# Performance work log

Measured on AMD Instinct MI355X. Metric: run time of the kernel, lower is better.

## Reference

```python
import jax, jax.numpy as jnp
import numpy as np

H, N, L = 512, 64, 2048


def setup_inputs() -> dict:
    key = jax.random.key(0)
    ks = jax.random.split(key, 9)
    x = jax.random.normal(ks[0], (L, H), jnp.float32)
    # HiPPO-style diagonal-plus-low-rank init (stable: Re(Lambda) < 0)
    lambda_re = -0.5 * jnp.ones((N,), jnp.float32)
    lambda_im = jnp.pi * jnp.arange(N, dtype=jnp.float32)
    p_re = jax.random.normal(ks[1], (N,), jnp.float32) / np.sqrt(2 * N)
    p_im = jax.random.normal(ks[2], (N,), jnp.float32) / np.sqrt(2 * N)
    b_re = jax.random.normal(ks[3], (N,), jnp.float32)
    b_im = jax.random.normal(ks[4], (N,), jnp.float32)
    c_re = jax.random.normal(ks[5], (N,), jnp.float32)
    c_im = jax.random.normal(ks[6], (N,), jnp.float32)
    log_step = jnp.array(np.log(0.01), jnp.float32)
    w1 = jax.random.normal(ks[7], (H, H), jnp.float32) / np.sqrt(H)
    bias1 = jnp.zeros((H,), jnp.float32)
    w2 = jax.random.normal(ks[8], (H, H), jnp.float32) / np.sqrt(H)
    bias2 = jnp.zeros((H,), jnp.float32)
    return dict(x=x, lambda_re=lambda_re, lambda_im=lambda_im, p_re=p_re, p_im=p_im,
                b_re=b_re, b_im=b_im, c_re=c_re, c_im=c_im, log_step=log_step,
                w1=w1, bias1=bias1, w2=w2, bias2=bias2)


def _discrete_dplr(Lam, P, B, C, step, seq_len):
    # Bilinear discretization of the DPLR SSM A = diag(Lam) - P P^* (annotated-S4).
    n = Lam.shape[0]
    I = jnp.eye(n, dtype=jnp.complex64)
    A = jnp.diag(Lam) - P[:, None] * jnp.conj(P)[None, :]
    A0 = (2.0 / step) * I + A
    Dd = jnp.diag(1.0 / (2.0 / step - Lam))  # (2/dt - Lam)^{-1} diagonal
    Qc = jnp.conj(P)[None, :]                 # (1, N)
    P2 = P[:, None]                           # (N, 1)
    A1 = Dd - (Dd @ P2) @ (Qc @ Dd) / (1.0 + (Qc @ Dd @ P2))  # Woodbury
    Ab = A1 @ A0                               # (N, N) discrete transition
    Bb = 2.0 * (A1 @ B[:, None])[:, 0]         # (N,)
    Cb = jnp.conj(
        C[None, :] @ jnp.conj(jnp.linalg.inv(I - jnp.linalg.matrix_power(Ab, seq_len)))
    )[0]                                       # (N,)
    return Ab, Bb, Cb


def reference(x, lambda_re, lambda_im, p_re, p_im, b_re, b_im, c_re, c_im,
              log_step, w1, bias1, w2, bias2):
    seq_len, hidden = x.shape
    Lam = (lambda_re + 1j * lambda_im).astype(jnp.complex64)
    P = (p_re + 1j * p_im).astype(jnp.complex64)
    B = (b_re + 1j * b_im).astype(jnp.complex64)
    C = (c_re + 1j * c_im).astype(jnp.complex64)
    step = jnp.exp(log_step)
    Ab, Bb, Cb = _discrete_dplr(Lam, P, B, C, step, seq_len)

    skip = x
    state0 = jnp.zeros((hidden, Lam.shape[0]), jnp.complex64)  # (H, N)

    def step_fn(state, u_l):  # u_l: (H,) real inputs at one timestep
        state = state @ Ab.T + u_l[:, None] * Bb[None, :]  # (H, N)
        y = (state @ Cb).real                               # (H,)
        return state, y

    _, ys = jax.lax.scan(step_fn, state0, x)  # ys: (L, H)
    h = jax.nn.gelu(ys)
    out = (h @ w1.T + bias1) * jax.nn.sigmoid(h @ w2.T + bias2)
    return skip + out
```

## Files before the change

### kernel.cpp

```cpp
#include <hip/hip_runtime.h>
#include <hip/hip_bf16.h>

typedef unsigned short u16;
typedef short s16x8 __attribute__((ext_vector_type(8)));
typedef u16 u16x8 __attribute__((ext_vector_type(8)));
typedef unsigned int u32x4 __attribute__((ext_vector_type(4)));
typedef float f32x4 __attribute__((ext_vector_type(4)));

struct cplx { float x, y; };

#define L_SEQ 2048
#define HID 512
#define NST 64

__device__ __align__(16) cplx g_khat[L_SEQ];
__device__ __align__(16) float g_k[L_SEQ];
__device__ __align__(16) u16 g_T[L_SEQ * L_SEQ];
__device__ __align__(16) u16 g_Xt[HID * L_SEQ];
__device__ __align__(16) u16 g_W1[HID * HID];
__device__ __align__(16) u16 g_W2[HID * HID];
__device__ __align__(16) u16 g_H[L_SEQ * HID];

__device__ __forceinline__ u16 f2bf(float f) {
    union { __hip_bfloat16 h; u16 u; } cv;
    cv.h = __float2bfloat16(f);
    return cv.u;
}

__global__ __launch_bounds__(256) void khat_kernel(
    const float* lre, const float* lim, const float* pre, const float* pim,
    const float* bre, const float* bim, const float* cre, const float* cim,
    const float* lstep) {
    __shared__ float sLre[NST], sLim[NST], sPre[NST], sPim[NST];
    __shared__ float sBre[NST], sBim[NST], sCre[NST], sCim[NST];
    int tid = threadIdx.x;
    if (tid < NST) {
        sLre[tid] = lre[tid]; sLim[tid] = lim[tid];
        sPre[tid] = pre[tid]; sPim[tid] = pim[tid];
        sBre[tid] = bre[tid]; sBim[tid] = bim[tid];
        sCre[tid] = cre[tid]; sCim[tid] = cim[tid];
    }
    __syncthreads();
    int j = blockIdx.x * 256 + tid;
    float tdt = 2.0f * __expf(-lstep[0]);
    float th = 0.00306796157577128245f * j;
    float sn, cs;
    __sincosf(th, &sn, &cs);
    float aRe = tdt * (1.f - cs), aIm = tdt * sn;
    float bRe = 1.f + cs, bIm = -sn;
    float cBx = 0.f, cBy = 0.f, cPx = 0.f, cPy = 0.f;
    float pBx = 0.f, pBy = 0.f, pPx = 0.f, pPy = 0.f;
#pragma unroll 8
    for (int n = 0; n < NST; n++) {
        float Lre = sLre[n], Lim = sLim[n];
        float Dre = aRe - (bRe * Lre - bIm * Lim);
        float Dim = aIm - (bRe * Lim + bIm * Lre);
        float inv = 1.f / (Dre * Dre + Dim * Dim);
        float eRe = Dre * inv, eIm = -Dim * inv;
        float cRe = sCre[n], cIm = -sCim[n];
        float t1Re = cRe * eRe - cIm * eIm, t1Im = cRe * eIm + cIm * eRe;
        float qRe = sPre[n], qIm = -sPim[n];
        float t2Re = qRe * eRe - qIm * eIm, t2Im = qRe * eIm + qIm * eRe;
        float BRe = sBre[n], BIm = sBim[n], PRe = sPre[n], PIm = sPim[n];
        cBx += t1Re * BRe - t1Im * BIm; cBy += t1Re * BIm + t1Im * BRe;
        cPx += t1Re * PRe - t1Im * PIm; cPy += t1Re * PIm + t1Im * PRe;
        pBx += t2Re * BRe - t2Im * BIm; pBy += t2Re * BIm + t2Im * BRe;
        pPx += t2Re * PRe - t2Im * PIm; pPy += t2Re * PIm + t2Im * PRe;
    }
    float denx = 1.f + (bRe * pPx - bIm * pPy);
    float deny = (bRe * pPy + bIm * pPx);
    float bcPx = bRe * cPx - bIm * cPy;
    float bcPy = bRe * cPy + bIm * cPx;
    float numx = bcPx * pBx - bcPy * pBy;
    float numy = bcPx * pBy + bcPy * pBx;
    float dinv = 1.f / (denx * denx + deny * deny);
    float corx = (numx * denx + numy * deny) * dinv;
    float cory = (numy * denx - numx * deny) * dinv;
    g_khat[j] = { 2.f * (cBx - corx), 2.f * (cBy - cory) };
}

__global__ __launch_bounds__(256) void k_ifft() {
    int tid = threadIdx.x;
    int l = tid & 63;
    int t = blockIdx.x * 4 + (tid >> 6);
    float acc = 0.f;
#pragma unroll
    for (int i = 0; i < 16; i++) {
        int j = l + 64 * i;
        cplx a = g_khat[j];
        cplx b = g_khat[(2048 - j) & 2047];
        float re = 0.5f * (a.x + b.x);
        float im = 0.5f * (a.y - b.y);
        int idx = (j * t) & 2047;
        float s, c;
        __sincosf(0.00306796157577128245f * idx, &s, &c);
        float wgt = (j == 0) ? 1.f : 2.f;
        acc += wgt * (re * c - im * s);
    }
    if (l == 0) {
        acc += (1 - 2 * (t & 1)) * g_khat[1024].x;
    }
#pragma unroll
    for (int off = 1; off < 64; off <<= 1) acc += __shfl_xor(acc, off);
    if (l == 0) g_k[t] = acc * (1.f / 2048.f);
}

__global__ __launch_bounds__(256) void fused_convert(const float* x, const float* w1,
                                                     const float* w2) {
    __shared__ float tile[64][65];
    int b = blockIdx.x, tid = threadIdx.x;
    if (b < 256) {
        int lt = b >> 3, ht = b & 7;
#pragma unroll
        for (int i = 0; i < 16; i++) {
            int idx = i * 256 + tid;
            int rr = idx >> 6, cc = idx & 63;
            tile[rr][cc] = x[(lt * 64 + rr) * HID + ht * 64 + cc];
        }
        __syncthreads();
#pragma unroll
        for (int i = 0; i < 16; i++) {
            int idx = i * 256 + tid;
            int rr = idx >> 6, cc = idx & 63;
            g_Xt[(ht * 64 + rr) * L_SEQ + lt * 64 + cc] = f2bf(tile[cc][rr]);
        }
    } else if (b < 768) {
        int t = (b - 256) * 256 + tid;
        const float* src = (t < 65536) ? w1 : w2;
        u16* dst = (t < 65536) ? g_W1 : g_W2;
        int idx = (t < 65536) ? t : (t - 65536);
        float4 v = ((const float4*)src)[idx];
        unsigned long long pk = (unsigned long long)f2bf(v.x) |
                                ((unsigned long long)f2bf(v.y) << 16) |
                                ((unsigned long long)f2bf(v.z) << 32) |
                                ((unsigned long long)f2bf(v.w) << 48);
        ((unsigned long long*)dst)[idx] = pk;
    } else {
        int gid = (b - 768) * 256 + tid;
        int o = gid * 8;
        int i = o >> 11, j0 = o & 2047;
        u16x8 v;
#pragma unroll
        for (int q = 0; q < 8; q++) {
            int d = i - (j0 + q);
            v[q] = f2bf((d >= 0) ? g_k[d] : 0.f);
        }
        *(u16x8*)&g_T[o] = v;
    }
}

__global__ __launch_bounds__(256) void conv_gemm() {
    __shared__ __align__(16) u16 As[64 * 64];
    __shared__ __align__(16) u16 Bs[64 * 64];
    int tid = threadIdx.x, l = tid & 63, w = tid >> 6;
    int wm = w >> 1, wn = w & 1;
    int bm = blockIdx.x >> 3, bn = blockIdx.x & 7;
    f32x4 acc[2][2] = {};
    int nkb = bm + 1;
    int row0 = tid >> 3, kc0 = tid & 7;
    int row1 = (256 + tid) >> 3, kc1 = tid & 7;
    const u16* arow0 = &g_T[(bm * 64 + row0) * L_SEQ + kc0 * 8];
    const u16* arow1 = &g_T[(bm * 64 + row1) * L_SEQ + kc1 * 8];
    const u16* brow0 = &g_Xt[(bn * 64 + row0) * L_SEQ + kc0 * 8];
    const u16* brow1 = &g_Xt[(bn * 64 + row1) * L_SEQ + kc1 * 8];
    int sa0 = row0 * 8 + (kc0 ^ (row0 & 7));
    int sa1 = row1 * 8 + (kc1 ^ (row1 & 7));
    u32x4 ra0 = *(const u32x4*)arow0;
    u32x4 ra1 = *(const u32x4*)arow1;
    u32x4 rb0 = *(const u32x4*)brow0;
    u32x4 rb1 = *(const u32x4*)brow1;
    for (int kb = 0; kb < nkb; kb++) {
        __syncthreads();
        ((u32x4*)As)[sa0] = ra0;
        ((u32x4*)As)[sa1] = ra1;
        ((u32x4*)Bs)[sa0] = rb0;
        ((u32x4*)Bs)[sa1] = rb1;
        if (kb + 1 < nkb) {
            int k0 = (kb + 1) * 64;
            ra0 = *(const u32x4*)(arow0 + k0);
            ra1 = *(const u32x4*)(arow1 + k0);
            rb0 = *(const u32x4*)(brow0 + k0);
            rb1 = *(const u32x4*)(brow1 + k0);
        }
        __syncthreads();
#pragma unroll
        for (int ks = 0; ks < 2; ks++) {
            s16x8 af[2], bf[2];
#pragma unroll
            for (int m = 0; m < 2; m++) {
                int row = wm * 32 + m * 16 + (l & 15);
                int chunk = (ks * 4 + (l >> 4)) ^ (row & 7);
                af[m] = *(const s16x8*)&As[row * 64 + chunk * 8];
            }
#pragma unroll
            for (int n = 0; n < 2; n++) {
                int col = wn * 32 + n * 16 + (l & 15);
                int chunk = (ks * 4 + (l >> 4)) ^ (col & 7);
                bf[n] = *(const s16x8*)&Bs[col * 64 + chunk * 8];
            }
#pragma unroll
            for (int m = 0; m < 2; m++)
#pragma unroll
                for (int n = 0; n < 2; n++)
                    acc[m][n] = __builtin_amdgcn_mfma_f32_16x16x32_bf16(af[m], bf[n], acc[m][n], 0, 0, 0);
        }
    }
#pragma unroll
    for (int m = 0; m < 2; m++)
#pragma unroll
        for (int n = 0; n < 2; n++)
#pragma unroll
            for (int r4 = 0; r4 < 4; r4++) {
                int row = bm * 64 + wm * 32 + m * 16 + (l >> 4) * 4 + r4;
                int col = bn * 64 + wn * 32 + n * 16 + (l & 15);
                float y = acc[m][n][r4];
                float u = 1.5957691216057308f * (y + 0.044715f * y * y * y);
                float th = 1.f - 2.f / (__expf(u) + 1.f);
                g_H[row * HID + col] = f2bf(0.5f * y * (1.f + th));
            }
}

__global__ __launch_bounds__(256) void ffn_gemm(const float* x, const float* b1,
                                                const float* b2, float* out) {
    __shared__ __align__(16) u16 As[64 * 64];
    __shared__ __align__(16) u16 B1s[64 * 64];
    __shared__ __align__(16) u16 B2s[64 * 64];
    int tid = threadIdx.x, l = tid & 63, w = tid >> 6;
    int wm = w >> 1, wn = w & 1;
    int bm = blockIdx.x >> 3, bn = blockIdx.x & 7;
    f32x4 acc1[2][2] = {}, acc2[2][2] = {};
    int row0 = tid >> 3, kc0 = tid & 7;
    int row1 = (256 + tid) >> 3;
    const u16* arow0 = &g_H[(bm * 64 + row0) * HID + kc0 * 8];
    const u16* arow1 = &g_H[(bm * 64 + row1) * HID + kc0 * 8];
    const u16* b1row0 = &g_W1[(bn * 64 + row0) * HID + kc0 * 8];
    const u16* b1row1 = &g_W1[(bn * 64 + row1) * HID + kc0 * 8];
    const u16* b2row0 = &g_W2[(bn * 64 + row0) * HID + kc0 * 8];
    const u16* b2row1 = &g_W2[(bn * 64 + row1) * HID + kc0 * 8];
    int sa0 = row0 * 8 + (kc0 ^ (row0 & 7));
    int sa1 = row1 * 8 + (kc0 ^ (row1 & 7));
    u32x4 ra0 = *(const u32x4*)arow0;
    u32x4 ra1 = *(const u32x4*)arow1;
    u32x4 rb10 = *(const u32x4*)b1row0;
    u32x4 rb11 = *(const u32x4*)b1row1;
    u32x4 rb20 = *(const u32x4*)b2row0;
    u32x4 rb21 = *(const u32x4*)b2row1;
    for (int kb = 0; kb < 8; kb++) {
        __syncthreads();
        ((u32x4*)As)[sa0] = ra0;
        ((u32x4*)As)[sa1] = ra1;
        ((u32x4*)B1s)[sa0] = rb10;
        ((u32x4*)B1s)[sa1] = rb11;
        ((u32x4*)B2s)[sa0] = rb20;
        ((u32x4*)B2s)[sa1] = rb21;
        if (kb < 7) {
            int k0 = (kb + 1) * 64;
            ra0 = *(const u32x4*)(arow0 + k0);
            ra1 = *(const u32x4*)(arow1 + k0);
            rb10 = *(const u32x4*)(b1row0 + k0);
            rb11 = *(const u32x4*)(b1row1 + k0);
            rb20 = *(const u32x4*)(b2row0 + k0);
            rb21 = *(const u32x4*)(b2row1 + k0);
        }
        __syncthreads();
#pragma unroll
        for (int ks = 0; ks < 2; ks++) {
            s16x8 af[2], b1f[2], b2f[2];
#pragma unroll
            for (int m = 0; m < 2; m++) {
                int row = wm * 32 + m * 16 + (l & 15);
                int chunk = (ks * 4 + (l >> 4)) ^ (row & 7);
                af[m] = *(const s16x8*)&As[row * 64 + chunk * 8];
            }
#pragma unroll
            for (int n = 0; n < 2; n++) {
                int col = wn * 32 + n * 16 + (l & 15);
                int chunk = (ks * 4 + (l >> 4)) ^ (col & 7);
                b1f[n] = *(const s16x8*)&B1s[col * 64 + chunk * 8];
                b2f[n] = *(const s16x8*)&B2s[col * 64 + chunk * 8];
            }
#pragma unroll
            for (int m = 0; m < 2; m++)
#pragma unroll
                for (int n = 0; n < 2; n++) {
                    acc1[m][n] = __builtin_amdgcn_mfma_f32_16x16x32_bf16(af[m], b1f[n], acc1[m][n], 0, 0, 0);
                    acc2[m][n] = __builtin_amdgcn_mfma_f32_16x16x32_bf16(af[m], b2f[n], acc2[m][n], 0, 0, 0);
                }
        }
    }
#pragma unroll
    for (int m = 0; m < 2; m++)
#pragma unroll
        for (int n = 0; n < 2; n++)
#pragma unroll
            for (int r4 = 0; r4 < 4; r4++) {
                int row = bm * 64 + wm * 32 + m * 16 + (l >> 4) * 4 + r4;
                int col = bn * 64 + wn * 32 + n * 16 + (l & 15);
                float g1 = acc1[m][n][r4] + b1[col];
                float g2 = acc2[m][n][r4] + b2[col];
                float sg = 1.f / (1.f + __expf(-g2));
                out[row * HID + col] = x[row * HID + col] + g1 * sg;
            }
}

extern "C" void kernel_launch(void* const* d_in, const int* in_sizes, int n_in,
                              void* d_out, int out_size, void* d_ws, size_t ws_size,
                              hipStream_t stream) {
    const float* x = (const float*)d_in[0];
    const float* lre = (const float*)d_in[1];
    const float* lim = (const float*)d_in[2];
    const float* pre = (const float*)d_in[3];
    const float* pim = (const float*)d_in[4];
    const float* bre = (const float*)d_in[5];
    const float* bim = (const float*)d_in[6];
    const float* cre = (const float*)d_in[7];
    const float* cim = (const float*)d_in[8];
    const float* lstep = (const float*)d_in[9];
    const float* w1 = (const float*)d_in[10];
    const float* b1 = (const float*)d_in[11];
    const float* w2 = (const float*)d_in[12];
    const float* b2 = (const float*)d_in[13];
    float* out = (float*)d_out;

    khat_kernel<<<8, 256, 0, stream>>>(lre, lim, pre, pim, bre, bim, cre, cim, lstep);
    k_ifft<<<512, 256, 0, stream>>>();
    fused_convert<<<2816, 256, 0, stream>>>(x, w1, w2);
    conv_gemm<<<256, 256, 0, stream>>>();
    ffn_gemm<<<256, 256, 0, stream>>>(x, b1, b2, out);
}
```

Before: 55.63 us.

## Build Toeplitz tiles on the fly in LDS and merge khat into convert kernel

Removes the materialized 2048x2048 bf16 Toeplitz matrix. conv_gemm now loads the kernel k into LDS and builds each A tile directly from it, which eliminates a large global write and read. The khat computation is folded into the convert kernel, cutting one launch. The x transpose is vectorized, and both GEMMs get a two-deep register prefetch. In exchange, each GEMM block does more ALU work and bf16 conversion per tile and uses more registers.

```diff
diff --git a/kernel.cpp b/kernel.cpp
--- a/kernel.cpp
+++ b/kernel.cpp
@@ -15,7 +15,6 @@
 
 __device__ __align__(16) cplx g_khat[L_SEQ];
 __device__ __align__(16) float g_k[L_SEQ];
-__device__ __align__(16) u16 g_T[L_SEQ * L_SEQ];
 __device__ __align__(16) u16 g_Xt[HID * L_SEQ];
 __device__ __align__(16) u16 g_W1[HID * HID];
 __device__ __align__(16) u16 g_W2[HID * HID];
@@ -27,102 +26,36 @@
     return cv.u;
 }
 
-__global__ __launch_bounds__(256) void khat_kernel(
+__global__ __launch_bounds__(256) void fused_convert(
+    const float* x, const float* w1, const float* w2,
     const float* lre, const float* lim, const float* pre, const float* pim,
     const float* bre, const float* bim, const float* cre, const float* cim,
     const float* lstep) {
+    __shared__ float tile[64][65];
     __shared__ float sLre[NST], sLim[NST], sPre[NST], sPim[NST];
     __shared__ float sBre[NST], sBim[NST], sCre[NST], sCim[NST];
-    int tid = threadIdx.x;
-    if (tid < NST) {
-        sLre[tid] = lre[tid]; sLim[tid] = lim[tid];
-        sPre[tid] = pre[tid]; sPim[tid] = pim[tid];
-        sBre[tid] = bre[tid]; sBim[tid] = bim[tid];
-        sCre[tid] = cre[tid]; sCim[tid] = cim[tid];
-    }
-    __syncthreads();
-    int j = blockIdx.x * 256 + tid;
-    float tdt = 2.0f * __expf(-lstep[0]);
-    float th = 0.00306796157577128245f * j;
-    float sn, cs;
-    __sincosf(th, &sn, &cs);
-    float aRe = tdt * (1.f - cs), aIm = tdt * sn;
-    float bRe = 1.f + cs, bIm = -sn;
-    float cBx = 0.f, cBy = 0.f, cPx = 0.f, cPy = 0.f;
-    float pBx = 0.f, pBy = 0.f, pPx = 0.f, pPy = 0.f;
-#pragma unroll 8
-    for (int n = 0; n < NST; n++) {
-        float Lre = sLre[n], Lim = sLim[n];
-        float Dre = aRe - (bRe * Lre - bIm * Lim);
-        float Dim = aIm - (bRe * Lim + bIm * Lre);
-        float inv = 1.f / (Dre * Dre + Dim * Dim);
-        float eRe = Dre * inv, eIm = -Dim * inv;
-        float cRe = sCre[n], cIm = -sCim[n];
-        float t1Re = cRe * eRe - cIm * eIm, t1Im = cRe * eIm + cIm * eRe;
-        float qRe = sPre[n], qIm = -sPim[n];
-        float t2Re = qRe * eRe - qIm * eIm, t2Im = qRe * eIm + qIm * eRe;
-        float BRe = sBre[n], BIm = sBim[n], PRe = sPre[n], PIm = sPim[n];
-        cBx += t1Re * BRe - t1Im * BIm; cBy += t1Re * BIm + t1Im * BRe;
-        cPx += t1Re * PRe - t1Im * PIm; cPy += t1Re * PIm + t1Im * PRe;
-        pBx += t2Re * BRe - t2Im * BIm; pBy += t2Re * BIm + t2Im * BRe;
-        pPx += t2Re * PRe - t2Im * PIm; pPy += t2Re * PIm + t2Im * PRe;
-    }
-    float denx = 1.f + (bRe * pPx - bIm * pPy);
-    float deny = (bRe * pPy + bIm * pPx);
-    float bcPx = bRe * cPx - bIm * cPy;
-    float bcPy = bRe * cPy + bIm * cPx;
-    float numx = bcPx * pBx - bcPy * pBy;
-    float numy = bcPx * pBy + bcPy * pBx;
-    float dinv = 1.f / (denx * denx + deny * deny);
-    float corx = (numx * denx + numy * deny) * dinv;
-    float cory = (numy * denx - numx * deny) * dinv;
-    g_khat[j] = { 2.f * (cBx - corx), 2.f * (cBy - cory) };
-}
-
-__global__ __launch_bounds__(256) void k_ifft() {
-    int tid = threadIdx.x;
-    int l = tid & 63;
-    int t = blockIdx.x * 4 + (tid >> 6);
-    float acc = 0.f;
-#pragma unroll
-    for (int i = 0; i < 16; i++) {
-        int j = l + 64 * i;
-        cplx a = g_khat[j];
-        cplx b = g_khat[(2048 - j) & 2047];
-        float re = 0.5f * (a.x + b.x);
-        float im = 0.5f * (a.y - b.y);
-        int idx = (j * t) & 2047;
-        float s, c;
-        __sincosf(0.00306796157577128245f * idx, &s, &c);
-        float wgt = (j == 0) ? 1.f : 2.f;
-        acc += wgt * (re * c - im * s);
-    }
-    if (l == 0) {
-        acc += (1 - 2 * (t & 1)) * g_khat[1024].x;
-    }
-#pragma unroll
-    for (int off = 1; off < 64; off <<= 1) acc += __shfl_xor(acc, off);
-    if (l == 0) g_k[t] = acc * (1.f / 2048.f);
-}
-
-__global__ __launch_bounds__(256) void fused_convert(const float* x, const float* w1,
-                                                     const float* w2) {
-    __shared__ float tile[64][65];
     int b = blockIdx.x, tid = threadIdx.x;
     if (b < 256) {
         int lt = b >> 3, ht = b & 7;
 #pragma unroll
-        for (int i = 0; i < 16; i++) {
+        for (int i = 0; i < 4; i++) {
             int idx = i * 256 + tid;
-            int rr = idx >> 6, cc = idx & 63;
-            tile[rr][cc] = x[(lt * 64 + rr) * HID + ht * 64 + cc];
+            int r = idx >> 4, c4 = idx & 15;
+            f32x4 v = *(const f32x4*)&x[(lt * 64 + r) * HID + ht * 64 + c4 * 4];
+            tile[r][c4 * 4 + 0] = v.x;
+            tile[r][c4 * 4 + 1] = v.y;
+            tile[r][c4 * 4 + 2] = v.z;
+            tile[r][c4 * 4 + 3] = v.w;
         }
         __syncthreads();
 #pragma unroll
-        for (int i = 0; i < 16; i++) {
+        for (int i = 0; i < 2; i++) {
             int idx = i * 256 + tid;
-            int rr = idx >> 6, cc = idx & 63;
-            g_Xt[(ht * 64 + rr) * L_SEQ + lt * 64 + cc] = f2bf(tile[cc][rr]);
+            int rr = idx >> 3, c8 = idx & 7;
+            u16x8 v;
+#pragma unroll
+            for (int q = 0; q < 8; q++) v[q] = f2bf(tile[c8 * 8 + q][rr]);
+            *(u16x8*)&g_Xt[(ht * 64 + rr) * L_SEQ + lt * 64 + c8 * 8] = v;
         }
     } else if (b < 768) {
         int t = (b - 256) * 256 + tid;
@@ -136,20 +69,78 @@
                                 ((unsigned long long)f2bf(v.w) << 48);
         ((unsigned long long*)dst)[idx] = pk;
     } else {
-        int gid = (b - 768) * 256 + tid;
-        int o = gid * 8;
-        int i = o >> 11, j0 = o & 2047;
-        u16x8 v;
-#pragma unroll
-        for (int q = 0; q < 8; q++) {
-            int d = i - (j0 + q);
-            v[q] = f2bf((d >= 0) ? g_k[d] : 0.f);
-        }
-        *(u16x8*)&g_T[o] = v;
-    }
+        if (tid < NST) {
+            sLre[tid] = lre[tid]; sLim[tid] = lim[tid];
+            sPre[tid] = pre[tid]; sPim[tid] = pim[tid];
+            sBre[tid] = bre[tid]; sBim[tid] = bim[tid];
+            sCre[tid] = cre[tid]; sCim[tid] = cim[tid];
+        }
+        __syncthreads();
+        int j = (b - 768) * 256 + tid;
+        float tdt = 2.0f * __expf(-lstep[0]);
+        float th = 0.00306796157577128245f * j;
+        float sn, cs;
+        __sincosf(th, &sn, &cs);
+        float aRe = tdt * (1.f - cs), aIm = tdt * sn;
+        float bRe = 1.f + cs, bIm = -sn;
+        float cBx = 0.f, cBy = 0.f, cPx = 0.f, cPy = 0.f;
+        float pBx = 0.f, pBy = 0.f, pPx = 0.f, pPy = 0.f;
+#pragma unroll 8
+        for (int n = 0; n < NST; n++) {
+            float Lre = sLre[n], Lim = sLim[n];
+            float Dre = aRe - (bRe * Lre - bIm * Lim);
+            float Dim = aIm - (bRe * Lim + bIm * Lre);
+            float inv = 1.f / (Dre * Dre + Dim * Dim);
+            float eRe = Dre * inv, eIm = -Dim * inv;
+            float cRe = sCre[n], cIm = -sCim[n];
+            float t1Re = cRe * eRe - cIm * eIm, t1Im = cRe * eIm + cIm * eRe;
+            float qRe = sPre[n], qIm = -sPim[n];
+            float t2Re = qRe * eRe - qIm * eIm, t2Im = qRe * eIm + qIm * eRe;
+            float BRe = sBre[n], BIm = sBim[n], PRe = sPre[n], PIm = sPim[n];
+            cBx += t1Re * BRe - t1Im * BIm; cBy += t1Re * BIm + t1Im * BRe;
+            cPx += t1Re * PRe - t1Im * PIm; cPy += t1Re * PIm + t1Im * PRe;
+            pBx += t2Re * BRe - t2Im * BIm; pBy += t2Re * BIm + t2Im * BRe;
+            pPx += t2Re * PRe - t2Im * PIm; pPy += t2Re * PIm + t2Im * PRe;
+        }
+        float denx = 1.f + (bRe * pPx - bIm * pPy);
+        float deny = (bRe * pPy + bIm * pPx);
+        float bcPx = bRe * cPx - bIm * cPy;
+        float bcPy = bRe * cPy + bIm * cPx;
+        float numx = bcPx * pBx - bcPy * pBy;
+        float numy = bcPx * pBy + bcPy * pBx;
+        float dinv = 1.f / (denx * denx + deny * deny);
+        float corx = (numx * denx + numy * deny) * dinv;
+        float cory = (numy * denx - numx * deny) * dinv;
+        g_khat[j] = { 2.f * (cBx - corx), 2.f * (cBy - cory) };
+    }
+}
+
+__global__ __launch_bounds__(256) void k_ifft() {
+    int tid = threadIdx.x;
+    int l = tid & 63;
+    int t = blockIdx.x * 4 + (tid >> 6);
+    float acc = 0.f;
+#pragma unroll
+    for (int i = 0; i < 16; i++) {
+        int j = l + 64 * i;
+        cplx a = g_khat[j];
+        cplx b = g_khat[(2048 - j) & 2047];
+        float re = 0.5f * (a.x + b.x);
+        float im = 0.5f * (a.y - b.y);
+        int idx = (j * t) & 2047;
+        float s, c;
+        __sincosf(0.00306796157577128245f * idx, &s, &c);
+        float wgt = (j == 0) ? 1.f : 2.f;
+        acc += wgt * (re * c - im * s);
+    }
+    if (l == 0) acc += (1 - 2 * (t & 1)) * g_khat[1024].x;
+#pragma unroll
+    for (int off = 1; off < 64; off <<= 1) acc += __shfl_xor(acc, off);
+    if (l == 0) g_k[t] = acc * (1.f / 2048.f);
 }
 
 __global__ __launch_bounds__(256) void conv_gemm() {
+    __shared__ __align__(16) float kLds[L_SEQ];
     __shared__ __align__(16) u16 As[64 * 64];
     __shared__ __align__(16) u16 Bs[64 * 64];
     int tid = threadIdx.x, l = tid & 63, w = tid >> 6;
@@ -159,52 +150,82 @@
     int nkb = bm + 1;
     int row0 = tid >> 3, kc0 = tid & 7;
     int row1 = (256 + tid) >> 3, kc1 = tid & 7;
-    const u16* arow0 = &g_T[(bm * 64 + row0) * L_SEQ + kc0 * 8];
-    const u16* arow1 = &g_T[(bm * 64 + row1) * L_SEQ + kc1 * 8];
     const u16* brow0 = &g_Xt[(bn * 64 + row0) * L_SEQ + kc0 * 8];
     const u16* brow1 = &g_Xt[(bn * 64 + row1) * L_SEQ + kc1 * 8];
     int sa0 = row0 * 8 + (kc0 ^ (row0 & 7));
     int sa1 = row1 * 8 + (kc1 ^ (row1 & 7));
-    u32x4 ra0 = *(const u32x4*)arow0;
-    u32x4 ra1 = *(const u32x4*)arow1;
-    u32x4 rb0 = *(const u32x4*)brow0;
-    u32x4 rb1 = *(const u32x4*)brow1;
-    for (int kb = 0; kb < nkb; kb++) {
-        __syncthreads();
-        ((u32x4*)As)[sa0] = ra0;
-        ((u32x4*)As)[sa1] = ra1;
-        ((u32x4*)Bs)[sa0] = rb0;
-        ((u32x4*)Bs)[sa1] = rb1;
-        if (kb + 1 < nkb) {
-            int k0 = (kb + 1) * 64;
-            ra0 = *(const u32x4*)(arow0 + k0);
-            ra1 = *(const u32x4*)(arow1 + k0);
-            rb0 = *(const u32x4*)(brow0 + k0);
-            rb1 = *(const u32x4*)(brow1 + k0);
-        }
-        __syncthreads();
-#pragma unroll
-        for (int ks = 0; ks < 2; ks++) {
-            s16x8 af[2], bf[2];
-#pragma unroll
-            for (int m = 0; m < 2; m++) {
-                int row = wm * 32 + m * 16 + (l & 15);
-                int chunk = (ks * 4 + (l >> 4)) ^ (row & 7);
-                af[m] = *(const s16x8*)&As[row * 64 + chunk * 8];
-            }
-#pragma unroll
-            for (int n = 0; n < 2; n++) {
-                int col = wn * 32 + n * 16 + (l & 15);
-                int chunk = (ks * 4 + (l >> 4)) ^ (col & 7);
-                bf[n] = *(const s16x8*)&Bs[col * 64 + chunk * 8];
-            }
-#pragma unroll
-            for (int m = 0; m < 2; m++)
-#pragma unroll
-                for (int n = 0; n < 2; n++)
-                    acc[m][n] = __builtin_amdgcn_mfma_f32_16x16x32_bf16(af[m], bf[n], acc[m][n], 0, 0, 0);
-        }
-    }
+#pragma unroll
+    for (int i = 0; i < 2; i++)
+        ((f32x4*)kLds)[i * 256 + tid] = ((const f32x4*)g_k)[i * 256 + tid];
+    u32x4 rbA0 = *(const u32x4*)brow0;
+    u32x4 rbA1 = *(const u32x4*)brow1;
+    u32x4 rbB0 = *(const u32x4*)(brow0 + 64);
+    u32x4 rbB1 = *(const u32x4*)(brow1 + 64);
+
+#define BUILD_AS(ROW, KC, SIDX)                                              \
+    {                                                                        \
+        int c0 = (KC) * 8;                                                   \
+        u16x8 av;                                                            \
+        _Pragma("unroll")                                                    \
+        for (int q = 0; q < 8; q++) {                                        \
+            int id = base + (ROW) - c0 - q;                                  \
+            av[q] = (id >= 0) ? f2bf(kLds[id]) : (u16)0;                     \
+        }                                                                    \
+        *(u16x8*)&As[(SIDX) * 8] = av;                                       \
+    }
+
+#define CONV_COMPUTE                                                         \
+    _Pragma("unroll")                                                        \
+    for (int ks = 0; ks < 2; ks++) {                                         \
+        s16x8 af[2], bf[2];                                                  \
+        _Pragma("unroll")                                                    \
+        for (int m = 0; m < 2; m++) {                                        \
+            int row = wm * 32 + m * 16 + (l & 15);                           \
+            int chunk = (ks * 4 + (l >> 4)) ^ (row & 7);                     \
+            af[m] = *(const s16x8*)&As[row * 64 + chunk * 8];                \
+        }                                                                    \
+        _Pragma("unroll")                                                    \
+        for (int n = 0; n < 2; n++) {                                        \
+            int col = wn * 32 + n * 16 + (l & 15);                           \
+            int chunk = (ks * 4 + (l >> 4)) ^ (col & 7);                     \
+            bf[n] = *(const s16x8*)&Bs[col * 64 + chunk * 8];                \
+        }                                                                    \
+        _Pragma("unroll")                                                    \
+        for (int m = 0; m < 2; m++)                                          \
+            _Pragma("unroll")                                                \
+            for (int n = 0; n < 2; n++)                                      \
+                acc[m][n] = __builtin_amdgcn_mfma_f32_16x16x32_bf16(         \
+                    af[m], bf[n], acc[m][n], 0, 0, 0);                       \
+    }
+
+#define CONV_STEP(R0, R1)                                                    \
+    {                                                                        \
+        __syncthreads();                                                     \
+        ((u32x4*)Bs)[sa0] = R0;                                              \
+        ((u32x4*)Bs)[sa1] = R1;                                              \
+        int base = (bm - kb) * 64;                                           \
+        BUILD_AS(row0, kc0, sa0);                                            \
+        BUILD_AS(row1, kc1, sa1);                                            \
+        if (kb + 2 < nkb) {                                                  \
+            int k0n = (kb + 2) * 64;                                         \
+            R0 = *(const u32x4*)(brow0 + k0n);                               \
+            R1 = *(const u32x4*)(brow1 + k0n);                               \
+        }                                                                    \
+        __syncthreads();                                                     \
+        CONV_COMPUTE;                                                        \
+        kb++;                                                                \
+    }
+
+    int kb = 0;
+    while (true) {
+        CONV_STEP(rbA0, rbA1);
+        if (kb >= nkb) break;
+        CONV_STEP(rbB0, rbB1);
+        if (kb >= nkb) break;
+    }
+#undef CONV_STEP
+#undef CONV_COMPUTE
+#undef BUILD_AS
 #pragma unroll
     for (int m = 0; m < 2; m++)
 #pragma unroll
@@ -239,28 +260,31 @@
     const u16* b2row1 = &g_W2[(bn * 64 + row1) * HID + kc0 * 8];
     int sa0 = row0 * 8 + (kc0 ^ (row0 & 7));
     int sa1 = row1 * 8 + (kc0 ^ (row1 & 7));
-    u32x4 ra0 = *(const u32x4*)arow0;
-    u32x4 ra1 = *(const u32x4*)arow1;
-    u32x4 rb10 = *(const u32x4*)b1row0;
-    u32x4 rb11 = *(const u32x4*)b1row1;
-    u32x4 rb20 = *(const u32x4*)b2row0;
-    u32x4 rb21 = *(const u32x4*)b2row1;
+    u32x4 rA0[2], rA1[2], rB10[2], rB11[2], rB20[2], rB21[2];
+    rA0[0] = *(const u32x4*)arow0;           rA0[1] = *(const u32x4*)(arow0 + 64);
+    rA1[0] = *(const u32x4*)arow1;           rA1[1] = *(const u32x4*)(arow1 + 64);
+    rB10[0] = *(const u32x4*)b1row0;         rB10[1] = *(const u32x4*)(b1row0 + 64);
+    rB11[0] = *(const u32x4*)b1row1;         rB11[1] = *(const u32x4*)(b1row1 + 64);
+    rB20[0] = *(const u32x4*)b2row0;         rB20[1] = *(const u32x4*)(b2row0 + 64);
+    rB21[0] = *(const u32x4*)b2row1;         rB21[1] = *(const u32x4*)(b2row1 + 64);
+#pragma unroll
     for (int kb = 0; kb < 8; kb++) {
+        const int cur = kb & 1;
         __syncthreads();
-        ((u32x4*)As)[sa0] = ra0;
-        ((u32x4*)As)[sa1] = ra1;
-        ((u32x4*)B1s)[sa0] = rb10;
-        ((u32x4*)B1s)[sa1] = rb11;
-        ((u32x4*)B2s)[sa0] = rb20;
-        ((u32x4*)B2s)[sa1] = rb21;
-        if (kb < 7) {
-            int k0 = (kb + 1) * 64;
-            ra0 = *(const u32x4*)(arow0 + k0);
-            ra1 = *(const u32x4*)(arow1 + k0);
-            rb10 = *(const u32x4*)(b1row0 + k0);
-            rb11 = *(const u32x4*)(b1row1 + k0);
-            rb20 = *(const u32x4*)(b2row0 + k0);
-            rb21 = *(const u32x4*)(b2row1 + k0);
+        ((u32x4*)As)[sa0] = rA0[cur];
+        ((u32x4*)As)[sa1] = rA1[cur];
+        ((u32x4*)B1s)[sa0] = rB10[cur];
+        ((u32x4*)B1s)[sa1] = rB11[cur];
+        ((u32x4*)B2s)[sa0] = rB20[cur];
+        ((u32x4*)B2s)[sa1] = rB21[cur];
+        if (kb + 2 < 8) {
+            int k0 = (kb + 2) * 64;
+            rA0[cur] = *(const u32x4*)(arow0 + k0);
+            rA1[cur] = *(const u32x4*)(arow1 + k0);
+            rB10[cur] = *(const u32x4*)(b1row0 + k0);
+            rB11[cur] = *(const u32x4*)(b1row1 + k0);
+            rB20[cur] = *(const u32x4*)(b2row0 + k0);
+            rB21[cur] = *(const u32x4*)(b2row1 + k0);
         }
         __syncthreads();
 #pragma unroll
@@ -322,9 +346,9 @@
     const float* b2 = (const float*)d_in[13];
     float* out = (float*)d_out;
 
-    khat_kernel<<<8, 256, 0, stream>>>(lre, lim, pre, pim, bre, bim, cre, cim, lstep);
+    fused_convert<<<776, 256, 0, stream>>>(x, w1, w2, lre, lim, pre, pim,
+                                           bre, bim, cre, cim, lstep);
     k_ifft<<<512, 256, 0, stream>>>();
-    fused_convert<<<2816, 256, 0, stream>>>(x, w1, w2);
     conv_gemm<<<256, 256, 0, stream>>>();
     ffn_gemm<<<256, 256, 0, stream>>>(x, b1, b2, out);
 }
```

Result: slower. 65.96 us (+18.6%).

## Replace dense Toeplitz matrix with per-diagonal 64x64 tiles and fuse prep kernels

Applied to the files above, without the earlier changes.

Drops the full 2048x2048 bf16 Toeplitz matrix and stores only 32 distinct 64x64 block tiles, since the Toeplitz block at (bm, kb) depends only on bm-kb. The k-generation (inverse DFT) now builds those tiles directly, and the khat computation is folded into the conversion kernel, cutting one launch and the large g_T write and read. The GEMMs switch to 64x32 tiles with twice as many blocks for more parallelism, and the x transpose uses vectorized loads and stores. The cost is more redundant A-tile loads per output column and more sincos work per k value in k_build.

```diff
diff --git a/kernel.cpp b/kernel.cpp
--- a/kernel.cpp
+++ b/kernel.cpp
@@ -14,8 +14,7 @@
 #define NST 64
 
 __device__ __align__(16) cplx g_khat[L_SEQ];
-__device__ __align__(16) float g_k[L_SEQ];
-__device__ __align__(16) u16 g_T[L_SEQ * L_SEQ];
+__device__ __align__(16) u16 g_Td[32 * 64 * 64];
 __device__ __align__(16) u16 g_Xt[HID * L_SEQ];
 __device__ __align__(16) u16 g_W1[HID * HID];
 __device__ __align__(16) u16 g_W2[HID * HID];
@@ -27,102 +26,36 @@
     return cv.u;
 }
 
-__global__ __launch_bounds__(256) void khat_kernel(
+__global__ __launch_bounds__(256) void fused_convert(
+    const float* x, const float* w1, const float* w2,
     const float* lre, const float* lim, const float* pre, const float* pim,
     const float* bre, const float* bim, const float* cre, const float* cim,
     const float* lstep) {
+    __shared__ float tile[64][65];
     __shared__ float sLre[NST], sLim[NST], sPre[NST], sPim[NST];
     __shared__ float sBre[NST], sBim[NST], sCre[NST], sCim[NST];
-    int tid = threadIdx.x;
-    if (tid < NST) {
-        sLre[tid] = lre[tid]; sLim[tid] = lim[tid];
-        sPre[tid] = pre[tid]; sPim[tid] = pim[tid];
-        sBre[tid] = bre[tid]; sBim[tid] = bim[tid];
-        sCre[tid] = cre[tid]; sCim[tid] = cim[tid];
-    }
-    __syncthreads();
-    int j = blockIdx.x * 256 + tid;
-    float tdt = 2.0f * __expf(-lstep[0]);
-    float th = 0.00306796157577128245f * j;
-    float sn, cs;
-    __sincosf(th, &sn, &cs);
-    float aRe = tdt * (1.f - cs), aIm = tdt * sn;
-    float bRe = 1.f + cs, bIm = -sn;
-    float cBx = 0.f, cBy = 0.f, cPx = 0.f, cPy = 0.f;
-    float pBx = 0.f, pBy = 0.f, pPx = 0.f, pPy = 0.f;
-#pragma unroll 8
-    for (int n = 0; n < NST; n++) {
-        float Lre = sLre[n], Lim = sLim[n];
-        float Dre = aRe - (bRe * Lre - bIm * Lim);
-        float Dim = aIm - (bRe * Lim + bIm * Lre);
-        float inv = 1.f / (Dre * Dre + Dim * Dim);
-        float eRe = Dre * inv, eIm = -Dim * inv;
-        float cRe = sCre[n], cIm = -sCim[n];
-        float t1Re = cRe * eRe - cIm * eIm, t1Im = cRe * eIm + cIm * eRe;
-        float qRe = sPre[n], qIm = -sPim[n];
-        float t2Re = qRe * eRe - qIm * eIm, t2Im = qRe * eIm + qIm * eRe;
-        float BRe = sBre[n], BIm = sBim[n], PRe = sPre[n], PIm = sPim[n];
-        cBx += t1Re * BRe - t1Im * BIm; cBy += t1Re * BIm + t1Im * BRe;
-        cPx += t1Re * PRe - t1Im * PIm; cPy += t1Re * PIm + t1Im * PRe;
-        pBx += t2Re * BRe - t2Im * BIm; pBy += t2Re * BIm + t2Im * BRe;
-        pPx += t2Re * PRe - t2Im * PIm; pPy += t2Re * PIm + t2Im * PRe;
-    }
-    float denx = 1.f + (bRe * pPx - bIm * pPy);
-    float deny = (bRe * pPy + bIm * pPx);
-    float bcPx = bRe * cPx - bIm * cPy;
-    float bcPy = bRe * cPy + bIm * cPx;
-    float numx = bcPx * pBx - bcPy * pBy;
-    float numy = bcPx * pBy + bcPy * pBx;
-    float dinv = 1.f / (denx * denx + deny * deny);
-    float corx = (numx * denx + numy * deny) * dinv;
-    float cory = (numy * denx - numx * deny) * dinv;
-    g_khat[j] = { 2.f * (cBx - corx), 2.f * (cBy - cory) };
-}
-
-__global__ __launch_bounds__(256) void k_ifft() {
-    int tid = threadIdx.x;
-    int l = tid & 63;
-    int t = blockIdx.x * 4 + (tid >> 6);
-    float acc = 0.f;
-#pragma unroll
-    for (int i = 0; i < 16; i++) {
-        int j = l + 64 * i;
-        cplx a = g_khat[j];
-        cplx b = g_khat[(2048 - j) & 2047];
-        float re = 0.5f * (a.x + b.x);
-        float im = 0.5f * (a.y - b.y);
-        int idx = (j * t) & 2047;
-        float s, c;
-        __sincosf(0.00306796157577128245f * idx, &s, &c);
-        float wgt = (j == 0) ? 1.f : 2.f;
-        acc += wgt * (re * c - im * s);
-    }
-    if (l == 0) {
-        acc += (1 - 2 * (t & 1)) * g_khat[1024].x;
-    }
-#pragma unroll
-    for (int off = 1; off < 64; off <<= 1) acc += __shfl_xor(acc, off);
-    if (l == 0) g_k[t] = acc * (1.f / 2048.f);
-}
-
-__global__ __launch_bounds__(256) void fused_convert(const float* x, const float* w1,
-                                                     const float* w2) {
-    __shared__ float tile[64][65];
     int b = blockIdx.x, tid = threadIdx.x;
     if (b < 256) {
         int lt = b >> 3, ht = b & 7;
 #pragma unroll
-        for (int i = 0; i < 16; i++) {
+        for (int i = 0; i < 4; i++) {
             int idx = i * 256 + tid;
-            int rr = idx >> 6, cc = idx & 63;
-            tile[rr][cc] = x[(lt * 64 + rr) * HID + ht * 64 + cc];
-        }
-        __syncthreads();
-#pragma unroll
-        for (int i = 0; i < 16; i++) {
+            int r = idx >> 4, c4 = idx & 15;
+            f32x4 v = *(const f32x4*)&x[(lt * 64 + r) * HID + ht * 64 + c4 * 4];
+            tile[r][c4 * 4 + 0] = v.x;
+            tile[r][c4 * 4 + 1] = v.y;
+            tile[r][c4 * 4 + 2] = v.z;
+            tile[r][c4 * 4 + 3] = v.w;
+        }
+        __syncthreads();
+#pragma unroll
+        for (int i = 0; i < 2; i++) {
             int idx = i * 256 + tid;
-            int rr = idx >> 6, cc = idx & 63;
-            g_Xt[(ht * 64 + rr) * L_SEQ + lt * 64 + cc] = f2bf(tile[cc][rr]);
+            int rr = idx >> 3, c8 = idx & 7;
+            u16x8 v;
+#pragma unroll
+            for (int q = 0; q < 8; q++) v[q] = f2bf(tile[c8 * 8 + q][rr]);
+            *(u16x8*)&g_Xt[(ht * 64 + rr) * L_SEQ + lt * 64 + c8 * 8] = v;
         }
     } else if (b < 768) {
         int t = (b - 256) * 256 + tid;
@@ -136,171 +69,222 @@
                                 ((unsigned long long)f2bf(v.w) << 48);
         ((unsigned long long*)dst)[idx] = pk;
     } else {
-        int gid = (b - 768) * 256 + tid;
-        int o = gid * 8;
-        int i = o >> 11, j0 = o & 2047;
-        u16x8 v;
-#pragma unroll
-        for (int q = 0; q < 8; q++) {
-            int d = i - (j0 + q);
-            v[q] = f2bf((d >= 0) ? g_k[d] : 0.f);
-        }
-        *(u16x8*)&g_T[o] = v;
+        if (tid < NST) {
+            sLre[tid] = lre[tid]; sLim[tid] = lim[tid];
+            sPre[tid] = pre[tid]; sPim[tid] = pim[tid];
+            sBre[tid] = bre[tid]; sBim[tid] = bim[tid];
+            sCre[tid] = cre[tid]; sCim[tid] = cim[tid];
+        }
+        __syncthreads();
+        int j = (b - 768) * 256 + tid;
+        float tdt = 2.0f * __expf(-lstep[0]);
+        float th = 0.00306796157577128245f * j;
+        float sn, cs;
+        __sincosf(th, &sn, &cs);
+        float aRe = tdt * (1.f - cs), aIm = tdt * sn;
+        float bRe = 1.f + cs, bIm = -sn;
+        float cBx = 0.f, cBy = 0.f, cPx = 0.f, cPy = 0.f;
+        float pBx = 0.f, pBy = 0.f, pPx = 0.f, pPy = 0.f;
+#pragma unroll 8
+        for (int n = 0; n < NST; n++) {
+            float Lre = sLre[n], Lim = sLim[n];
+            float Dre = aRe - (bRe * Lre - bIm * Lim);
+            float Dim = aIm - (bRe * Lim + bIm * Lre);
+            float inv = 1.f / (Dre * Dre + Dim * Dim);
+            float eRe = Dre * inv, eIm = -Dim * inv;
+            float cRe = sCre[n], cIm = -sCim[n];
+            float t1Re = cRe * eRe - cIm * eIm, t1Im = cRe * eIm + cIm * eRe;
+            float qRe = sPre[n], qIm = -sPim[n];
+            float t2Re = qRe * eRe - qIm * eIm, t2Im = qRe * eIm + qIm * eRe;
+            float BRe = sBre[n], BIm = sBim[n], PRe = sPre[n], PIm = sPim[n];
+            cBx += t1Re * BRe - t1Im * BIm; cBy += t1Re * BIm + t1Im * BRe;
+            cPx += t1Re * PRe - t1Im * PIm; cPy += t1Re * PIm + t1Im * PRe;
+            pBx += t2Re * BRe - t2Im * BIm; pBy += t2Re * BIm + t2Im * BRe;
+            pPx += t2Re * PRe - t2Im * PIm; pPy += t2Re * PIm + t2Im * PRe;
+        }
+        float denx = 1.f + (bRe * pPx - bIm * pPy);
+        float deny = (bRe * pPy + bIm * pPx);
+        float bcPx = bRe * cPx - bIm * cPy;
+        float bcPy = bRe * cPy + bIm * cPx;
+        float numx = bcPx * pBx - bcPy * pBy;
+        float numy = bcPx * pBy + bcPy * pBx;
+        float dinv = 1.f / (denx * denx + deny * deny);
+        float corx = (numx * denx + numy * deny) * dinv;
+        float cory = (numy * denx - numx * deny) * dinv;
+        g_khat[j] = { 2.f * (cBx - corx), 2.f * (cBy - cory) };
+    }
+}
+
+__global__ __launch_bounds__(256) void k_build() {
+    int d = blockIdx.x >> 3, s = blockIdx.x & 7;
+    int tid = threadIdx.x;
+    int gv = tid >> 4, p = tid & 15;
+    int v = s * 16 + gv;
+    int o = v - 63;
+    int t = 64 * d + o;
+    float acc = 0.f;
+#pragma unroll 8
+    for (int i = 0; i < 64; i++) {
+        int j = p + 16 * i;
+        cplx a = g_khat[j];
+        cplx b = g_khat[(2048 - j) & 2047];
+        float re = 0.5f * (a.x + b.x);
+        float im = 0.5f * (a.y - b.y);
+        int idx = (j * t) & 2047;
+        float sn, cs;
+        __sincosf(0.00306796157577128245f * idx, &sn, &cs);
+        acc += ((j == 0) ? 1.f : 2.f) * (re * cs - im * sn);
+    }
+    acc += __shfl_xor(acc, 1);
+    acc += __shfl_xor(acc, 2);
+    acc += __shfl_xor(acc, 4);
+    acc += __shfl_xor(acc, 8);
+    float kv = 0.f;
+    if (t >= 0) kv = (acc + (1 - 2 * (t & 1)) * g_khat[1024].x) * (1.f / 2048.f);
+    u16 kb16 = f2bf(kv);
+    int ao = (o >= 0) ? o : -o;
+    int len = 64 - ao;
+#pragma unroll
+    for (int q = 0; q < 4; q++) {
+        int e = p * 4 + q;
+        if (e < len) {
+            int r = (o >= 0) ? e + o : e;
+            int c = r - o;
+            g_Td[d * 4096 + r * 64 + c] = kb16;
+        }
     }
 }
 
 __global__ __launch_bounds__(256) void conv_gemm() {
     __shared__ __align__(16) u16 As[64 * 64];
-    __shared__ __align__(16) u16 Bs[64 * 64];
+    __shared__ __align__(16) u16 Bs[32 * 64];
     int tid = threadIdx.x, l = tid & 63, w = tid >> 6;
     int wm = w >> 1, wn = w & 1;
-    int bm = blockIdx.x >> 3, bn = blockIdx.x & 7;
-    f32x4 acc[2][2] = {};
+    int bm = blockIdx.x >> 4, bn = blockIdx.x & 15;
+    f32x4 acc[2] = {};
     int nkb = bm + 1;
     int row0 = tid >> 3, kc0 = tid & 7;
-    int row1 = (256 + tid) >> 3, kc1 = tid & 7;
-    const u16* arow0 = &g_T[(bm * 64 + row0) * L_SEQ + kc0 * 8];
-    const u16* arow1 = &g_T[(bm * 64 + row1) * L_SEQ + kc1 * 8];
-    const u16* brow0 = &g_Xt[(bn * 64 + row0) * L_SEQ + kc0 * 8];
-    const u16* brow1 = &g_Xt[(bn * 64 + row1) * L_SEQ + kc1 * 8];
+    int row1 = row0 + 32;
     int sa0 = row0 * 8 + (kc0 ^ (row0 & 7));
-    int sa1 = row1 * 8 + (kc1 ^ (row1 & 7));
-    u32x4 ra0 = *(const u32x4*)arow0;
-    u32x4 ra1 = *(const u32x4*)arow1;
-    u32x4 rb0 = *(const u32x4*)brow0;
-    u32x4 rb1 = *(const u32x4*)brow1;
+    int sa1 = row1 * 8 + (kc0 ^ (row1 & 7));
+    const u16* aB0 = &g_Td[bm * 4096 + row0 * 64 + kc0 * 8];
+    const u16* aB1 = &g_Td[bm * 4096 + row1 * 64 + kc0 * 8];
+    const u16* bB0 = &g_Xt[(bn * 32 + row0) * L_SEQ + kc0 * 8];
+    u32x4 ra0 = *(const u32x4*)aB0;
+    u32x4 ra1 = *(const u32x4*)aB1;
+    u32x4 rb0 = *(const u32x4*)bB0;
     for (int kb = 0; kb < nkb; kb++) {
         __syncthreads();
         ((u32x4*)As)[sa0] = ra0;
         ((u32x4*)As)[sa1] = ra1;
         ((u32x4*)Bs)[sa0] = rb0;
-        ((u32x4*)Bs)[sa1] = rb1;
         if (kb + 1 < nkb) {
-            int k0 = (kb + 1) * 64;
-            ra0 = *(const u32x4*)(arow0 + k0);
-            ra1 = *(const u32x4*)(arow1 + k0);
-            rb0 = *(const u32x4*)(brow0 + k0);
-            rb1 = *(const u32x4*)(brow1 + k0);
+            ra0 = *(const u32x4*)(aB0 - (kb + 1) * 4096);
+            ra1 = *(const u32x4*)(aB1 - (kb + 1) * 4096);
+            rb0 = *(const u32x4*)(bB0 + (kb + 1) * 64);
         }
         __syncthreads();
 #pragma unroll
         for (int ks = 0; ks < 2; ks++) {
-            s16x8 af[2], bf[2];
+            s16x8 af[2], bf;
 #pragma unroll
             for (int m = 0; m < 2; m++) {
                 int row = wm * 32 + m * 16 + (l & 15);
-                int chunk = (ks * 4 + (l >> 4)) ^ (row & 7);
-                af[m] = *(const s16x8*)&As[row * 64 + chunk * 8];
-            }
-#pragma unroll
-            for (int n = 0; n < 2; n++) {
-                int col = wn * 32 + n * 16 + (l & 15);
-                int chunk = (ks * 4 + (l >> 4)) ^ (col & 7);
-                bf[n] = *(const s16x8*)&Bs[col * 64 + chunk * 8];
+                int ch = (ks * 4 + (l >> 4)) ^ (row & 7);
+                af[m] = *(const s16x8*)&As[row * 64 + ch * 8];
+            }
+            {
+                int col = wn * 16 + (l & 15);
+                int ch = (ks * 4 + (l >> 4)) ^ (col & 7);
+                bf = *(const s16x8*)&Bs[col * 64 + ch * 8];
             }
 #pragma unroll
             for (int m = 0; m < 2; m++)
-#pragma unroll
-                for (int n = 0; n < 2; n++)
-                    acc[m][n] = __builtin_amdgcn_mfma_f32_16x16x32_bf16(af[m], bf[n], acc[m][n], 0, 0, 0);
+                acc[m] = __builtin_amdgcn_mfma_f32_16x16x32_bf16(af[m], bf, acc[m], 0, 0, 0);
         }
     }
 #pragma unroll
     for (int m = 0; m < 2; m++)
 #pragma unroll
-        for (int n = 0; n < 2; n++)
-#pragma unroll
-            for (int r4 = 0; r4 < 4; r4++) {
-                int row = bm * 64 + wm * 32 + m * 16 + (l >> 4) * 4 + r4;
-                int col = bn * 64 + wn * 32 + n * 16 + (l & 15);
-                float y = acc[m][n][r4];
-                float u = 1.5957691216057308f * (y + 0.044715f * y * y * y);
-                float th = 1.f - 2.f / (__expf(u) + 1.f);
-                g_H[row * HID + col] = f2bf(0.5f * y * (1.f + th));
-            }
+        for (int r4 = 0; r4 < 4; r4++) {
+            int row = bm * 64 + wm * 32 + m * 16 + (l >> 4) * 4 + r4;
+            int col = bn * 32 + wn * 16 + (l & 15);
+            float y = acc[m][r4];
+            float uu = 1.5957691216057308f * (y + 0.044715f * y * y * y);
+            float th = 1.f - 2.f / (__expf(uu) + 1.f);
+            g_H[row * HID + col] = f2bf(0.5f * y * (1.f + th));
+        }
 }
 
 __global__ __launch_bounds__(256) void ffn_gemm(const float* x, const float* b1,
                                                 const float* b2, float* out) {
     __shared__ __align__(16) u16 As[64 * 64];
-    __shared__ __align__(16) u16 B1s[64 * 64];
-    __shared__ __align__(16) u16 B2s[64 * 64];
+    __shared__ __align__(16) u16 B1s[32 * 64];
+    __shared__ __align__(16) u16 B2s[32 * 64];
     int tid = threadIdx.x, l = tid & 63, w = tid >> 6;
     int wm = w >> 1, wn = w & 1;
-    int bm = blockIdx.x >> 3, bn = blockIdx.x & 7;
-    f32x4 acc1[2][2] = {}, acc2[2][2] = {};
+    int bm = blockIdx.x >> 4, bn = blockIdx.x & 15;
+    f32x4 acc1[2] = {}, acc2[2] = {};
     int row0 = tid >> 3, kc0 = tid & 7;
-    int row1 = (256 + tid) >> 3;
-    const u16* arow0 = &g_H[(bm * 64 + row0) * HID + kc0 * 8];
-    const u16* arow1 = &g_H[(bm * 64 + row1) * HID + kc0 * 8];
-    const u16* b1row0 = &g_W1[(bn * 64 + row0) * HID + kc0 * 8];
-    const u16* b1row1 = &g_W1[(bn * 64 + row1) * HID + kc0 * 8];
-    const u16* b2row0 = &g_W2[(bn * 64 + row0) * HID + kc0 * 8];
-    const u16* b2row1 = &g_W2[(bn * 64 + row1) * HID + kc0 * 8];
+    int row1 = row0 + 32;
     int sa0 = row0 * 8 + (kc0 ^ (row0 & 7));
     int sa1 = row1 * 8 + (kc0 ^ (row1 & 7));
-    u32x4 ra0 = *(const u32x4*)arow0;
-    u32x4 ra1 = *(const u32x4*)arow1;
-    u32x4 rb10 = *(const u32x4*)b1row0;
-    u32x4 rb11 = *(const u32x4*)b1row1;
-    u32x4 rb20 = *(const u32x4*)b2row0;
-    u32x4 rb21 = *(const u32x4*)b2row1;
+    const u16* aB0 = &g_H[(bm * 64 + row0) * HID + kc0 * 8];
+    const u16* aB1 = &g_H[(bm * 64 + row1) * HID + kc0 * 8];
+    const u16* w1B = &g_W1[(bn * 32 + row0) * HID + kc0 * 8];
+    const u16* w2B = &g_W2[(bn * 32 + row0) * HID + kc0 * 8];
+    u32x4 ra0 = *(const u32x4*)aB0;
+    u32x4 ra1 = *(const u32x4*)aB1;
+    u32x4 r1 = *(const u32x4*)w1B;
+    u32x4 r2 = *(const u32x4*)w2B;
+#pragma unroll
     for (int kb = 0; kb < 8; kb++) {
         __syncthreads();
         ((u32x4*)As)[sa0] = ra0;
         ((u32x4*)As)[sa1] = ra1;
-        ((u32x4*)B1s)[sa0] = rb10;
-        ((u32x4*)B1s)[sa1] = rb11;
-        ((u32x4*)B2s)[sa0] = rb20;
-        ((u32x4*)B2s)[sa1] = rb21;
+        ((u32x4*)B1s)[sa0] = r1;
+        ((u32x4*)B2s)[sa0] = r2;
         if (kb < 7) {
             int k0 = (kb + 1) * 64;
-            ra0 = *(const u32x4*)(arow0 + k0);
-            ra1 = *(const u32x4*)(arow1 + k0);
-            rb10 = *(const u32x4*)(b1row0 + k0);
-            rb11 = *(const u32x4*)(b1row1 + k0);
-            rb20 = *(const u32x4*)(b2row0 + k0);
-            rb21 = *(const u32x4*)(b2row1 + k0);
+            ra0 = *(const u32x4*)(aB0 + k0);
+            ra1 = *(const u32x4*)(aB1 + k0);
+            r1 = *(const u32x4*)(w1B + k0);
+            r2 = *(const u32x4*)(w2B + k0);
         }
         __syncthreads();
 #pragma unroll
         for (int ks = 0; ks < 2; ks++) {
-            s16x8 af[2], b1f[2], b2f[2];
+            s16x8 af[2], b1f, b2f;
 #pragma unroll
             for (int m = 0; m < 2; m++) {
                 int row = wm * 32 + m * 16 + (l & 15);
-                int chunk = (ks * 4 + (l >> 4)) ^ (row & 7);
-                af[m] = *(const s16x8*)&As[row * 64 + chunk * 8];
-            }
-#pragma unroll
-            for (int n = 0; n < 2; n++) {
-                int col = wn * 32 + n * 16 + (l & 15);
-                int chunk = (ks * 4 + (l >> 4)) ^ (col & 7);
-                b1f[n] = *(const s16x8*)&B1s[col * 64 + chunk * 8];
-                b2f[n] = *(const s16x8*)&B2s[col * 64 + chunk * 8];
-            }
-#pragma unroll
-            for (int m = 0; m < 2; m++)
-#pragma unroll
-                for (int n = 0; n < 2; n++) {
-                    acc1[m][n] = __builtin_amdgcn_mfma_f32_16x16x32_bf16(af[m], b1f[n], acc1[m][n], 0, 0, 0);
-                    acc2[m][n] = __builtin_amdgcn_mfma_f32_16x16x32_bf16(af[m], b2f[n], acc2[m][n], 0, 0, 0);
-                }
+                int ch = (ks * 4 + (l >> 4)) ^ (row & 7);
+                af[m] = *(const s16x8*)&As[row * 64 + ch * 8];
+            }
+            {
+                int col = wn * 16 + (l & 15);
+                int ch = (ks * 4 + (l >> 4)) ^ (col & 7);
+                b1f = *(const s16x8*)&B1s[col * 64 + ch * 8];
+                b2f = *(const s16x8*)&B2s[col * 64 + ch * 8];
+            }
+#pragma unroll
+            for (int m = 0; m < 2; m++) {
+                acc1[m] = __builtin_amdgcn_mfma_f32_16x16x32_bf16(af[m], b1f, acc1[m], 0, 0, 0);
+                acc2[m] = __builtin_amdgcn_mfma_f32_16x16x32_bf16(af[m], b2f, acc2[m], 0, 0, 0);
+            }
         }
     }
 #pragma unroll
     for (int m = 0; m < 2; m++)
 #pragma unroll
-        for (int n = 0; n < 2; n++)
-#pragma unroll
-            for (int r4 = 0; r4 < 4; r4++) {
-                int row = bm * 64 + wm * 32 + m * 16 + (l >> 4) * 4 + r4;
-                int col = bn * 64 + wn * 32 + n * 16 + (l & 15);
-                float g1 = acc1[m][n][r4] + b1[col];
-                float g2 = acc2[m][n][r4] + b2[col];
-                float sg = 1.f / (1.f + __expf(-g2));
-                out[row * HID + col] = x[row * HID + col] + g1 * sg;
-            }
+        for (int r4 = 0; r4 < 4; r4++) {
+            int row = bm * 64 + wm * 32 + m * 16 + (l >> 4) * 4 + r4;
+            int col = bn * 32 + wn * 16 + (l & 15);
+            float g1 = acc1[m][r4] + b1[col];
+            float g2 = acc2[m][r4] + b2[col];
+            float sg = 1.f / (1.f + __expf(-g2));
+            out[row * HID + col] = x[row * HID + col] + g1 * sg;
+        }
 }
 
 extern "C" void kernel_launch(void* const* d_in, const int* in_sizes, int n_in,
@@ -322,9 +306,9 @@
     const float* b2 = (const float*)d_in[13];
     float* out = (float*)d_out;
 
-    khat_kernel<<<8, 256, 0, stream>>>(lre, lim, pre, pim, bre, bim, cre, cim, lstep);
-    k_ifft<<<512, 256, 0, stream>>>();
-    fused_convert<<<2816, 256, 0, stream>>>(x, w1, w2);
-    conv_gemm<<<256, 256, 0, stream>>>();
-    ffn_gemm<<<256, 256, 0, stream>>>(x, b1, b2, out);
-}
+    fused_convert<<<776, 256, 0, stream>>>(x, w1, w2, lre, lim, pre, pim,
+                                           bre, bim, cre, cim, lstep);
+    k_build<<<256, 256, 0, stream>>>();
+    conv_gemm<<<512, 256, 0, stream>>>();
+    ffn_gemm<<<512, 256, 0, stream>>>(x, b1, b2, out);
+}
```

Measured after the change: 62.38 us. 1.12x slower.
